# Kernel optimization log

Measured on AMD Instinct MI355X. Metric: run time of the kernel, lower is better.

## Reference

```python
import jax, jax.numpy as jnp
import numpy as np

N, C, E, H = 50000, 128, 1_600_000, 32
JITTER = 1e-20


def _lin(k, fan_in, fan_out):
    return jax.random.normal(k, (fan_in, fan_out), jnp.float32) / np.sqrt(fan_in)


def setup_inputs() -> dict:
    key = jax.random.key(0)
    ks = jax.random.split(key, 20)
    x = jax.random.normal(ks[0], (N, C), jnp.float32)
    edge_index = jax.random.randint(ks[1], (2, E), 0, N, dtype=jnp.int64)
    inp = {"x": x, "edge_index": edge_index}
    # actor params
    inp["aW"] = _lin(ks[2], C, C); inp["ab"] = jnp.zeros((C,), jnp.float32)
    inp["a1W"] = _lin(ks[3], C, H); inp["a1b"] = jnp.zeros((H,), jnp.float32)
    inp["a2W"] = _lin(ks[4], H, H); inp["a2b"] = jnp.zeros((H,), jnp.float32)
    inp["a3W"] = _lin(ks[5], H, 2); inp["a3b"] = jnp.zeros((2,), jnp.float32)
    # critic params
    inp["cW"] = _lin(ks[6], C, C); inp["cb"] = jnp.zeros((C,), jnp.float32)
    inp["c1W"] = _lin(ks[7], C, H); inp["c1b"] = jnp.zeros((H,), jnp.float32)
    inp["c2W"] = _lin(ks[8], H, H); inp["c2b"] = jnp.zeros((H,), jnp.float32)
    inp["c3W"] = _lin(ks[9], H, 2); inp["c3b"] = jnp.zeros((2,), jnp.float32)
    return inp


def gcn_conv(x, src, dst, W, b):
    """Standard PyG GCNConv: add self-loops, symmetric degree norm, X@W, scatter-add, +bias."""
    n = x.shape[0]
    loop = jnp.arange(n)
    s = jnp.concatenate([src, loop])  # [E+N]
    d = jnp.concatenate([dst, loop])
    deg = jax.ops.segment_sum(jnp.ones_like(d, jnp.float32), d, num_segments=n)
    dinv = jnp.where(deg > 0, jax.lax.rsqrt(deg), 0.0)
    norm = dinv[s] * dinv[d]                     # [E+N]
    h = x @ W                                    # [N, C]
    agg = jax.ops.segment_sum(h[s] * norm[:, None], d, num_segments=n)
    return agg + b


def reference(x, edge_index, aW, ab, a1W, a1b, a2W, a2b, a3W, a3b,
              cW, cb, c1W, c1b, c2W, c2b, c3W, c3b):
    src, dst = edge_index[0], edge_index[1]
    # actor
    h = jax.nn.relu(gcn_conv(x, src, dst, aW, ab)) + x
    h = jax.nn.relu(h @ a1W + a1b)
    h = jax.nn.relu(h @ a2W + a2b)
    a = h @ a3W + a3b                            # [N, 2]
    concentration = jax.nn.softplus(a[:, 0]) + JITTER
    p = jax.nn.softplus(a[:, 1])
    action2_probs = p / jnp.sum(p)
    # critic
    hc = jax.nn.relu(gcn_conv(x, src, dst, cW, cb)) + x
    hc = jnp.sum(hc, axis=0)                     # [C]
    hc = jax.nn.relu(hc @ c1W + c1b)
    hc = jax.nn.relu(hc @ c2W + c2b)
    value = hc @ c3W + c3b                       # [2]
    return (concentration, value, action2_probs)
```

## Files before the change

### kernel.cpp

```cpp
#include <hip/hip_runtime.h>
#include <hip/hip_bf16.h>
#include <hip/hip_fp16.h>
#include <math.h>

#define C 128
#define BCAP 12288

using half8x = __attribute__((ext_vector_type(8))) _Float16;
using half4x = __attribute__((ext_vector_type(4))) _Float16;
using f32x4  = __attribute__((ext_vector_type(4))) float;

__device__ inline float4 h4_to_f4(uint2 u) {
    __half2 p0 = *(__half2*)&u.x;
    __half2 p1 = *(__half2*)&u.y;
    float2 f0 = __half22float2(p0), f1 = __half22float2(p1);
    return make_float4(f0.x, f0.y, f1.x, f1.y);
}

__device__ inline float softplusf(float v) {
    return (v > 20.f) ? v : log1pf(expf(v));
}

__global__ __launch_bounds__(256) void initk(unsigned* gcur, float* colsum, float* pSum) {
    int t = threadIdx.x;
    gcur[t] = 0u;
    if (t < 128) colsum[t] = 0.f;
    if (t == 128) pSum[0] = 0.f;
}

__global__ __launch_bounds__(256) void wtk(const float* __restrict__ aW, const float* __restrict__ cW,
                                           const float* __restrict__ a1W,
                                           __half* __restrict__ wt, __half* __restrict__ a1wt) {
    int idx = blockIdx.x * 256 + threadIdx.x;
    if (idx < 32768) {
        int y = idx >> 14, r = idx & 16383;
        int k = r >> 7, n = r & 127;
        const float* W = y ? cW : aW;
        wt[((size_t)y << 14) + n * 128 + k] = __float2half(W[k * 128 + n]);
    } else if (idx < 36864) {
        int r = idx - 32768;
        int k = r >> 5, n = r & 31;
        a1wt[n * 128 + k] = __float2half(a1W[k * 32 + n]);
    }
}

__global__ __launch_bounds__(256) void bink(const int* __restrict__ ei,
                                            unsigned* __restrict__ gcur,
                                            unsigned* __restrict__ gstage,
                                            int E, int NBKT) {
    __shared__ unsigned raw[6400];
    __shared__ unsigned image[6400];
    __shared__ unsigned cnt[256];
    __shared__ unsigned pref[256];
    __shared__ unsigned cur[256];
    __shared__ unsigned gb[256];
    int t = threadIdx.x, b = blockIdx.x;
    int elo = (int)((long long)b * E / 256);
    int ehi = (int)((long long)(b + 1) * E / 256);
    int n = ehi - elo;

    for (int i = t; i < n; i += 256) {
        int d = __builtin_nontemporal_load(ei + E + elo + i);
        int s = __builtin_nontemporal_load(ei + elo + i);
        raw[i] = (unsigned)s | ((unsigned)(d & 255) << 16) | ((unsigned)(d >> 8) << 24);
    }
    cnt[t] = 0u; cur[t] = 0u;
    __syncthreads();
    for (int i = t; i < n; i += 256) atomicAdd(&cnt[raw[i] >> 24], 1u);
    __syncthreads();
    pref[t] = cnt[t];
    __syncthreads();
    for (int off = 1; off < 256; off <<= 1) {
        unsigned add = (t >= off) ? pref[t - off] : 0u;
        __syncthreads();
        pref[t] += add;
        __syncthreads();
    }
    gb[t] = (t < NBKT && cnt[t]) ? atomicAdd(&gcur[t], cnt[t]) : 0u;
    __syncthreads();
    for (int i = t; i < n; i += 256) {
        unsigned v = raw[i];
        unsigned B = v >> 24;
        unsigned pos = (pref[B] - cnt[B]) + atomicAdd(&cur[B], 1u);
        image[pos] = v & 0xFFFFFFu;
    }
    __syncthreads();
    int wv = t >> 6, lane = t & 63;
    for (int B = wv; B < NBKT; B += 4) {
        unsigned c = cnt[B];
        if (!c) continue;
        unsigned eb = pref[B] - c;
        unsigned gbase = gb[B];
        unsigned c2 = (gbase < BCAP) ? ((c < BCAP - gbase) ? c : BCAP - gbase) : 0u;
        for (unsigned i = lane; i < c2; i += 64)
            gstage[(size_t)B * BCAP + gbase + i] = image[eb + i];
    }
}

__global__ void bktscank(const unsigned* __restrict__ gcur, unsigned* __restrict__ bktbase, int NBKT) {
    __shared__ unsigned tmp[256];
    int t = threadIdx.x;
    unsigned g = (t < NBKT) ? gcur[t] : 0u;
    unsigned v = (g < BCAP) ? g : BCAP;
    tmp[t] = v;
    __syncthreads();
    for (int off = 1; off < 256; off <<= 1) {
        unsigned add = (t >= off) ? tmp[t - off] : 0u;
        __syncthreads();
        tmp[t] += add;
        __syncthreads();
    }
    if (t < NBKT) bktbase[t] = tmp[t] - v;
}

__global__ __launch_bounds__(256) void placek(const unsigned* __restrict__ gstage,
                                              const unsigned* __restrict__ gcur,
                                              const unsigned* __restrict__ bktbase,
                                              int* __restrict__ rowptr, float* __restrict__ dinv,
                                              int* __restrict__ col, int N, int NBKT) {
    __shared__ unsigned image[BCAP];
    __shared__ unsigned cnt[256];
    __shared__ unsigned pref[256];
    __shared__ unsigned cur[256];
    int B = blockIdx.x, t = threadIdx.x;
    unsigned g = gcur[B];
    unsigned m = (g < BCAP) ? g : BCAP;
    unsigned base = bktbase[B];
    const unsigned* st = gstage + (size_t)B * BCAP;

    cnt[t] = 0u; cur[t] = 0u;
    __syncthreads();
    for (unsigned i = t; i < m; i += 256) atomicAdd(&cnt[(st[i] >> 16) & 255u], 1u);
    __syncthreads();
    pref[t] = cnt[t];
    __syncthreads();
    for (int off = 1; off < 256; off <<= 1) {
        unsigned add = (t >= off) ? pref[t - off] : 0u;
        __syncthreads();
        pref[t] += add;
        __syncthreads();
    }
    int d = B * 256 + t;
    if (d < N) {
        rowptr[d] = (int)(base + pref[t] - cnt[t]);
        dinv[d] = rsqrtf((float)(cnt[t] + 1u));
    }
    if (B == NBKT - 1 && t == 0) rowptr[N] = (int)(base + m);
    for (unsigned i = t; i < m; i += 256) {
        unsigned v = st[i];
        unsigned dl = (v >> 16) & 255u;
        unsigned pos = (pref[dl] - cnt[dl]) + atomicAdd(&cur[dl], 1u);
        image[pos] = v & 0xFFFFu;
    }
    __syncthreads();
    for (unsigned i = t; i < m; i += 256) col[base + i] = (int)image[i];
}

__global__ __launch_bounds__(256) void xhk(const float* __restrict__ x, const float* __restrict__ dinv,
                                           __half* __restrict__ xh, __half* __restrict__ x16, int N) {
    int i = blockIdx.x * 256 + threadIdx.x;
    if (i >= N * 64) return;
    int node = i >> 6, fp = (i & 63) * 2;
    float w = dinv[node];
    float2 f = *(const float2*)&x[(size_t)node * C + fp];
    __half2 h = __floats2half2_rn(f.x * w, f.y * w);
    __half2 hx = __floats2half2_rn(f.x, f.y);
    *(unsigned*)&xh[(size_t)node * C + fp] = *(unsigned*)&h;
    *(unsigned*)&x16[(size_t)node * C + fp] = *(unsigned*)&hx;
}

__global__ __launch_bounds__(256) void gatherk(const int* __restrict__ col,
                                               const int* __restrict__ rowptr,
                                               const __half* __restrict__ xh,
                                               const float* __restrict__ dinv,
                                               __half* __restrict__ gg, int N) {
    __shared__ int snb[4][64];
    int t = threadIdx.x;
    int wid = t >> 6, lane = t & 63;
    int d = blockIdx.x * 4 + wid;
    if (d >= N) return;
    int beg = rowptr[d], end = rowptr[d + 1];
    int half = lane >> 5, sub = lane & 31;
    int f = sub * 4;

    float a0 = 0.f, a1 = 0.f, a2 = 0.f, a3 = 0.f;

    for (int c = beg; c < end; c += 64) {
        if (c + lane < end) snb[wid][lane] = col[c + lane];
        int n = end - c; if (n > 64) n = 64;
        int j = 0;
        for (; j + 3 < n; j += 4) {
            size_t i0 = (size_t)snb[wid][j + half] * C + f;
            size_t i1 = (size_t)snb[wid][j + 2 + half] * C + f;
            float4 v0 = h4_to_f4(*(const uint2*)&xh[i0]);
            float4 v1 = h4_to_f4(*(const uint2*)&xh[i1]);
            a0 += v0.x + v1.x;
            a1 += v0.y + v1.y;
            a2 += v0.z + v1.z;
            a3 += v0.w + v1.w;
        }
        for (; j < n; j += 2) {
            if (j + half < n) {
                float4 v = h4_to_f4(*(const uint2*)&xh[(size_t)snb[wid][j + half] * C + f]);
                a0 += v.x; a1 += v.y; a2 += v.z; a3 += v.w;
            }
        }
    }
    a0 += __shfl_xor(a0, 32, 64);
    a1 += __shfl_xor(a1, 32, 64);
    a2 += __shfl_xor(a2, 32, 64);
    a3 += __shfl_xor(a3, 32, 64);

    if (half == 0) {
        float4 s4 = h4_to_f4(*(const uint2*)&xh[(size_t)d * C + f]);
        float dv = dinv[d];
        __half2 h0 = __floats2half2_rn((a0 + s4.x) * dv, (a1 + s4.y) * dv);
        __half2 h1 = __floats2half2_rn((a2 + s4.z) * dv, (a3 + s4.w) * dv);
        uint2 u; u.x = *(unsigned*)&h0; u.y = *(unsigned*)&h1;
        *(uint2*)&gg[(size_t)d * C + f] = u;
    }
}

__global__ __launch_bounds__(256) void gemm2k(const __half* __restrict__ gg,
                                              const __half* __restrict__ wt,
                                              const __half* __restrict__ a1wt,
                                              const float* __restrict__ ab, const float* __restrict__ cb,
                                              const __half* __restrict__ x16,
                                              const float* __restrict__ a1b,
                                              const float* __restrict__ a2W, const float* __restrict__ a2b,
                                              const float* __restrict__ a3W, const float* __restrict__ a3b,
                                              float* __restrict__ scratch,
                                              float* __restrict__ out, float* __restrict__ pSum, int N) {
    __shared__ char As[16384];
    __shared__ char Aux[10240];
    _Float16* w2t = (_Float16*)Aux;
    _Float16* h1b = (_Float16*)(Aux + 2560);
    float* w3s    = (float*)(Aux + 7680);
    float* scol   = (float*)(Aux + 7936);

    const int row0 = blockIdx.x * 64;
    const int t = threadIdx.x;

#pragma unroll
    for (int i = 0; i < 4; ++i) {
        int c = t + i * 256;
        int row = c >> 4, cb16 = (c & 15) * 16;
        int grow = row0 + row;
        uint4 u = make_uint4(0u, 0u, 0u, 0u);
        if (grow < N) u = *(const uint4*)&gg[(size_t)grow * C + (c & 15) * 8];
        *(uint4*)(As + row * 256 + (cb16 ^ ((row & 7) << 4))) = u;
    }
#pragma unroll
    for (int i = 0; i < 4; ++i) {
        int idx = t + i * 256;
        int k = idx >> 5, n = idx & 31;
        w2t[n * 40 + k] = (_Float16)a2W[idx];
    }
    if (t < 64) w3s[t] = a3W[t];
    __syncthreads();

    int wv = t >> 6, l = t & 63;
    int lm = l & 15, lk = l >> 4;
    int koffB = lk * 16;
    int koffH = lk * 8;

    const int rowA = wv * 16 + lm;
    const int grow = row0 + rowA;
    const bool valid = grow < N;
    const int sw = (rowA & 7) << 4;

    half8x af[4];
    {
        const char* rp = As + rowA * 256;
#pragma unroll
        for (int kc = 0; kc < 4; ++kc)
            af[kc] = *(const half8x*)(rp + ((kc * 64 + koffB) ^ sw));
    }

    const __half* WA = wt;
    const __half* WC = wt + 16384;

    half8x bfA[4], bfC[4];
    {
        const __half* wpA = WA + lm * 128;
        const __half* wpC = WC + lm * 128;
#pragma unroll
        for (int kc = 0; kc < 4; ++kc) {
            bfA[kc] = *(const half8x*)(wpA + kc * 32 + koffH);
            bfC[kc] = *(const half8x*)(wpC + kc * 32 + koffH);
        }
    }

#pragma unroll
    for (int nc = 0; nc < 8; ++nc) {
        half8x nA[4], nC[4];
        if (nc < 7) {
            const __half* wpA = WA + ((nc + 1) * 16 + lm) * 128;
            const __half* wpC = WC + ((nc + 1) * 16 + lm) * 128;
#pragma unroll
            for (int kc = 0; kc < 4; ++kc) {
                nA[kc] = *(const half8x*)(wpA + kc * 32 + koffH);
                nC[kc] = *(const half8x*)(wpC + kc * 32 + koffH);
            }
        }
        f32x4 accA = {0.f, 0.f, 0.f, 0.f};
        f32x4 accC = {0.f, 0.f, 0.f, 0.f};
#pragma unroll
        for (int kc = 0; kc < 4; ++kc) {
            accA = __builtin_amdgcn_mfma_f32_16x16x32_f16(bfA[kc], af[kc], accA, 0, 0, 0);
            accC = __builtin_amdgcn_mfma_f32_16x16x32_f16(bfC[kc], af[kc], accC, 0, 0, 0);
        }
        float4 bvA = *(const float4*)&ab[nc * 16 + lk * 4];
        float4 bvC = *(const float4*)&cb[nc * 16 + lk * 4];
        half4x xq = {};
        if (valid) xq = *(const half4x*)&x16[(size_t)grow * C + nc * 16 + lk * 4];
        {
            half4x hv = { (_Float16)(valid ? fmaxf(accA[0] + bvA.x, 0.f) + (float)xq[0] : 0.f),
                          (_Float16)(valid ? fmaxf(accA[1] + bvA.y, 0.f) + (float)xq[1] : 0.f),
                          (_Float16)(valid ? fmaxf(accA[2] + bvA.z, 0.f) + (float)xq[2] : 0.f),
                          (_Float16)(valid ? fmaxf(accA[3] + bvA.w, 0.f) + (float)xq[3] : 0.f) };
            *(half4x*)(As + rowA * 256 + ((nc * 32 + lk * 8) ^ sw)) = hv;
        }
        {
            float v0 = valid ? fmaxf(accC[0] + bvC.x, 0.f) + (float)xq[0] : 0.f;
            float v1 = valid ? fmaxf(accC[1] + bvC.y, 0.f) + (float)xq[1] : 0.f;
            float v2 = valid ? fmaxf(accC[2] + bvC.z, 0.f) + (float)xq[2] : 0.f;
            float v3 = valid ? fmaxf(accC[3] + bvC.w, 0.f) + (float)xq[3] : 0.f;
            v0 += __shfl_xor(v0, 1, 64); v0 += __shfl_xor(v0, 2, 64);
            v0 += __shfl_xor(v0, 4, 64); v0 += __shfl_xor(v0, 8, 64);
            v1 += __shfl_xor(v1, 1, 64); v1 += __shfl_xor(v1, 2, 64);
            v1 += __shfl_xor(v1, 4, 64); v1 += __shfl_xor(v1, 8, 64);
            v2 += __shfl_xor(v2, 1, 64); v2 += __shfl_xor(v2, 2, 64);
            v2 += __shfl_xor(v2, 4, 64); v2 += __shfl_xor(v2, 8, 64);
            v3 += __shfl_xor(v3, 1, 64); v3 += __shfl_xor(v3, 2, 64);
            v3 += __shfl_xor(v3, 4, 64); v3 += __shfl_xor(v3, 8, 64);
            if (lm == 0)
                *(float4*)&scol[wv * 128 + nc * 16 + lk * 4] = make_float4(v0, v1, v2, v3);
        }
        if (nc < 7) {
#pragma unroll
            for (int kc = 0; kc < 4; ++kc) { bfA[kc] = nA[kc]; bfC[kc] = nC[kc]; }
        }
    }
    __syncthreads();

    if (t < 128)
        scratch[(size_t)blockIdx.x * 128 + t] = scol[t] + scol[128 + t] + scol[256 + t] + scol[384 + t];

    half8x a1f[4];
    {
        const char* rp = As + rowA * 256;
#pragma unroll
        for (int kc = 0; kc < 4; ++kc)
            a1f[kc] = *(const half8x*)(rp + ((kc * 64 + koffB) ^ sw));
    }
#pragma unroll
    for (int ct = 0; ct < 2; ++ct) {
        const __half* ap = a1wt + (ct * 16 + lm) * 128;
        f32x4 acc1 = {0.f, 0.f, 0.f, 0.f};
#pragma unroll
        for (int kc = 0; kc < 4; ++kc) {
            half8x bq = *(const half8x*)(ap + kc * 32 + koffH);
            acc1 = __builtin_amdgcn_mfma_f32_16x16x32_f16(bq, a1f[kc], acc1, 0, 0, 0);
        }
        float4 b1v = *(const float4*)&a1b[ct * 16 + lk * 4];
        half4x h = { (_Float16)fmaxf(acc1[0] + b1v.x, 0.f),
                     (_Float16)fmaxf(acc1[1] + b1v.y, 0.f),
                     (_Float16)fmaxf(acc1[2] + b1v.z, 0.f),
                     (_Float16)fmaxf(acc1[3] + b1v.w, 0.f) };
        *(half4x*)((char*)h1b + rowA * 80 + ct * 32 + lk * 8) = h;
    }

    half4x alo = *(const half4x*)((char*)h1b + rowA * 80 + lk * 16);
    half4x ahi = *(const half4x*)((char*)h1b + rowA * 80 + lk * 16 + 8);
    half8x a2f = __builtin_shufflevector(alo, ahi, 0, 1, 2, 3, 4, 5, 6, 7);
    float p0 = 0.f, p1 = 0.f;
#pragma unroll
    for (int ct = 0; ct < 2; ++ct) {
        half4x blo = *(const half4x*)((char*)w2t + (ct * 16 + lm) * 80 + lk * 16);
        half4x bhi = *(const half4x*)((char*)w2t + (ct * 16 + lm) * 80 + lk * 16 + 8);
        half8x b2f = __builtin_shufflevector(blo, bhi, 0, 1, 2, 3, 4, 5, 6, 7);
        f32x4 acc2 = {0.f, 0.f, 0.f, 0.f};
        acc2 = __builtin_amdgcn_mfma_f32_16x16x32_f16(b2f, a2f, acc2, 0, 0, 0);
        float4 b2v = *(const float4*)&a2b[ct * 16 + lk * 4];
#pragma unroll
        for (int j = 0; j < 4; ++j) {
            int f = ct * 16 + lk * 4 + j;
            float h2v = fmaxf(acc2[j] + (&b2v.x)[j], 0.f);
            float2 w3 = *(const float2*)&w3s[f * 2];
            p0 += h2v * w3.x;
            p1 += h2v * w3.y;
        }
    }
    p0 += __shfl_xor(p0, 16, 64); p0 += __shfl_xor(p0, 32, 64);
    p1 += __shfl_xor(p1, 16, 64); p1 += __shfl_xor(p1, 32, 64);
    float wave_psum = 0.f;
    if (lk == 0 && valid) {
        float s0 = softplusf(p0 + a3b[0]);
        float s1 = softplusf(p1 + a3b[1]);
        out[grow] = s0 + 1e-20f;
        out[(size_t)N + 2 + grow] = s1;
        wave_psum = s1;
    }
    wave_psum += __shfl_xor(wave_psum, 1, 64);
    wave_psum += __shfl_xor(wave_psum, 2, 64);
    wave_psum += __shfl_xor(wave_psum, 4, 64);
    wave_psum += __shfl_xor(wave_psum, 8, 64);
    wave_psum += __shfl_xor(wave_psum, 16, 64);
    wave_psum += __shfl_xor(wave_psum, 32, 64);
    if (l == 0) atomicAdd(pSum, wave_psum);
}

__global__ __launch_bounds__(128) void csredk(const float* __restrict__ scratch, float* __restrict__ colsum, int nblk) {
    int t = threadIdx.x;
    float s = 0.f;
    for (int b = blockIdx.x; b < nblk; b += gridDim.x)
        s += scratch[(size_t)b * 128 + t];
    atomicAdd(&colsum[t], s);
}

__global__ void critick(const float* __restrict__ colsum,
                        const float* __restrict__ c1W, const float* __restrict__ c1b,
                        const float* __restrict__ c2W, const float* __restrict__ c2b,
                        const float* __restrict__ c3W, const float* __restrict__ c3b,
                        float* __restrict__ out, int N) {
    __shared__ float s1[32], s2[32];
    int t = threadIdx.x;
    if (t < 32) {
        float acc = c1b[t];
        for (int k = 0; k < 128; ++k) acc += colsum[k] * c1W[k * 32 + t];
        s1[t] = fmaxf(acc, 0.f);
    }
    __syncthreads();
    if (t < 32) {
        float acc = c2b[t];
        for (int k = 0; k < 32; ++k) acc += s1[k] * c2W[k * 32 + t];
        s2[t] = fmaxf(acc, 0.f);
    }
    __syncthreads();
    if (t < 2) {
        float acc = c3b[t];
        for (int k = 0; k < 32; ++k) acc += s2[k] * c3W[k * 2 + t];
        out[(size_t)N + t] = acc;
    }
}

__global__ __launch_bounds__(256) void normk(float* __restrict__ out, const float* __restrict__ pSum, int N) {
    int i = blockIdx.x * 256 + threadIdx.x;
    if (i < N) out[(size_t)N + 2 + i] /= pSum[0];
}

extern "C" void kernel_launch(void* const* d_in, const int* in_sizes, int n_in,
                              void* d_out, int out_size, void* d_ws, size_t ws_size,
                              hipStream_t stream) {
    const float* x   = (const float*)d_in[0];
    const int* ei    = (const int*)d_in[1];
    const float* aW  = (const float*)d_in[2];
    const float* ab  = (const float*)d_in[3];
    const float* a1W = (const float*)d_in[4];
    const float* a1b = (const float*)d_in[5];
    const float* a2W = (const float*)d_in[6];
    const float* a2b = (const float*)d_in[7];
    const float* a3W = (const float*)d_in[8];
    const float* a3b = (const float*)d_in[9];
    const float* cW  = (const float*)d_in[10];
    const float* cb  = (const float*)d_in[11];
    const float* c1W = (const float*)d_in[12];
    const float* c1b = (const float*)d_in[13];
    const float* c2W = (const float*)d_in[14];
    const float* c2b = (const float*)d_in[15];
    const float* c3W = (const float*)d_in[16];
    const float* c3b = (const float*)d_in[17];

    const int N = in_sizes[0] / C;
    const int E = in_sizes[1] / 2;
    const int NBKT = (N + 255) / 256;
    const int nblk64 = (N + 63) / 64;
    float* out = (float*)d_out;

    char* ws = (char*)d_ws;
    size_t off = 0;
    auto alloc = [&](size_t bytes) {
        size_t o = off;
        off = (off + bytes + 255) & ~(size_t)255;
        return (void*)(ws + o);
    };
    unsigned* gcur    = (unsigned*)alloc(256 * 4);
    unsigned* bktbase = (unsigned*)alloc(256 * 4);
    unsigned* gstage  = (unsigned*)alloc((size_t)NBKT * BCAP * 4);
    int* rowptr       = (int*)alloc((size_t)(N + 1) * 4);
    float* dinv       = (float*)alloc((size_t)N * 4);
    int* colidx       = (int*)alloc((size_t)E * 4);
    __half* xh        = (__half*)alloc((size_t)N * C * 2);
    __half* x16       = (__half*)alloc((size_t)N * C * 2);
    __half* gg        = (__half*)alloc((size_t)N * C * 2);
    __half* wt        = (__half*)alloc(2 * 16384 * 2);
    __half* a1wt      = (__half*)alloc(4096 * 2);
    float* scratch    = (float*)alloc((size_t)nblk64 * 128 * 4);
    float* colsum     = (float*)alloc(128 * 4);
    float* pSum       = (float*)alloc(4);

    initk<<<1, 256, 0, stream>>>(gcur, colsum, pSum);
    wtk<<<144, 256, 0, stream>>>(aW, cW, a1W, wt, a1wt);
    bink<<<256, 256, 0, stream>>>(ei, gcur, gstage, E, NBKT);
    bktscank<<<1, 256, 0, stream>>>(gcur, bktbase, NBKT);
    placek<<<NBKT, 256, 0, stream>>>(gstage, gcur, bktbase, rowptr, dinv, colidx, N, NBKT);
    xhk<<<(N * 64 + 255) / 256, 256, 0, stream>>>(x, dinv, xh, x16, N);
    gatherk<<<(N + 3) / 4, 256, 0, stream>>>(colidx, rowptr, xh, dinv, gg, N);
    gemm2k<<<nblk64, 256, 0, stream>>>(gg, wt, a1wt, ab, cb, x16,
                                       a1b, a2W, a2b, a3W, a3b,
                                       scratch, out, pSum, N);
    csredk<<<8, 128, 0, stream>>>(scratch, colsum, nblk64);
    critick<<<1, 64, 0, stream>>>(colsum, c1W, c1b, c2W, c2b, c3W, c3b, out, N);
    normk<<<(N + 255) / 256, 256, 0, stream>>>(out, pSum, N);
}
```

Measured before the change: 228.1 us.

## Split gemm2 output columns across waves instead of rows to cut weight loads

In gemm2k, each wave used to own 16 rows and loop over all 8 column chunks, which meant every wave streamed the full WA and WC weight matrices from global memory. Now each wave owns 2 column chunks and loops over all 64 rows, so each wave loads only a quarter of the weights, and A fragments are read from LDS inside the loop. The result goes into a separate Act LDS buffer to avoid read/write conflicts on As. This raises LDS use and LDS reads per wave, and it drops the software prefetch of the next weight chunk.

New measurement: 217.7 us. 1.05x faster.

```diff
diff --git a/kernel.cpp b/kernel.cpp
--- a/kernel.cpp
+++ b/kernel.cpp
@@ -232,7 +232,8 @@
                                               float* __restrict__ scratch,
                                               float* __restrict__ out, float* __restrict__ pSum, int N) {
     __shared__ char As[16384];
-    __shared__ char Aux[10240];
+    __shared__ char Act[16384];
+    __shared__ char Aux[8448];
     _Float16* w2t = (_Float16*)Aux;
     _Float16* h1b = (_Float16*)(Aux + 2560);
     float* w3s    = (float*)(Aux + 7680);
@@ -264,95 +265,78 @@
     int koffB = lk * 16;
     int koffH = lk * 8;
 
-    const int rowA = wv * 16 + lm;
-    const int grow = row0 + rowA;
-    const bool valid = grow < N;
-    const int sw = (rowA & 7) << 4;
-
-    half8x af[4];
-    {
-        const char* rp = As + rowA * 256;
-#pragma unroll
-        for (int kc = 0; kc < 4; ++kc)
-            af[kc] = *(const half8x*)(rp + ((kc * 64 + koffB) ^ sw));
-    }
-
     const __half* WA = wt;
     const __half* WC = wt + 16384;
 
-    half8x bfA[4], bfC[4];
-    {
-        const __half* wpA = WA + lm * 128;
-        const __half* wpC = WC + lm * 128;
+#pragma unroll
+    for (int nc2 = 0; nc2 < 2; ++nc2) {
+        const int nc = wv * 2 + nc2;
+        const __half* wpA = WA + (nc * 16 + lm) * 128;
+        const __half* wpC = WC + (nc * 16 + lm) * 128;
+        half8x bfA[4], bfC[4];
 #pragma unroll
         for (int kc = 0; kc < 4; ++kc) {
             bfA[kc] = *(const half8x*)(wpA + kc * 32 + koffH);
             bfC[kc] = *(const half8x*)(wpC + kc * 32 + koffH);
         }
-    }
-
-#pragma unroll
-    for (int nc = 0; nc < 8; ++nc) {
-        half8x nA[4], nC[4];
-        if (nc < 7) {
-            const __half* wpA = WA + ((nc + 1) * 16 + lm) * 128;
-            const __half* wpC = WC + ((nc + 1) * 16 + lm) * 128;
-#pragma unroll
-            for (int kc = 0; kc < 4; ++kc) {
-                nA[kc] = *(const half8x*)(wpA + kc * 32 + koffH);
-                nC[kc] = *(const half8x*)(wpC + kc * 32 + koffH);
-            }
-        }
-        f32x4 accA = {0.f, 0.f, 0.f, 0.f};
-        f32x4 accC = {0.f, 0.f, 0.f, 0.f};
-#pragma unroll
-        for (int kc = 0; kc < 4; ++kc) {
-            accA = __builtin_amdgcn_mfma_f32_16x16x32_f16(bfA[kc], af[kc], accA, 0, 0, 0);
-            accC = __builtin_amdgcn_mfma_f32_16x16x32_f16(bfC[kc], af[kc], accC, 0, 0, 0);
-        }
         float4 bvA = *(const float4*)&ab[nc * 16 + lk * 4];
         float4 bvC = *(const float4*)&cb[nc * 16 + lk * 4];
-        half4x xq = {};
-        if (valid) xq = *(const half4x*)&x16[(size_t)grow * C + nc * 16 + lk * 4];
-        {
+        float v0 = 0.f, v1 = 0.f, v2 = 0.f, v3 = 0.f;
+
+#pragma unroll
+        for (int rg = 0; rg < 4; ++rg) {
+            int rowA = rg * 16 + lm;
+            int grow = row0 + rowA;
+            bool valid = grow < N;
+            int sw = (rowA & 7) << 4;
+            const char* rp = As + rowA * 256;
+            f32x4 accA = {0.f, 0.f, 0.f, 0.f};
+            f32x4 accC = {0.f, 0.f, 0.f, 0.f};
+#pragma unroll
+            for (int kc = 0; kc < 4; ++kc) {
+                half8x afr = *(const half8x*)(rp + ((kc * 64 + koffB) ^ sw));
+                accA = __builtin_amdgcn_mfma_f32_16x16x32_f16(bfA[kc], afr, accA, 0, 0, 0);
+                accC = __builtin_amdgcn_mfma_f32_16x16x32_f16(bfC[kc], afr, accC, 0, 0, 0);
+            }
+            half4x xq = {};
+            if (valid) xq = *(const half4x*)&x16[(size_t)grow * C + nc * 16 + lk * 4];
             half4x hv = { (_Float16)(valid ? fmaxf(accA[0] + bvA.x, 0.f) + (float)xq[0] : 0.f),
                           (_Float16)(valid ? fmaxf(accA[1] + bvA.y, 0.f) + (float)xq[1] : 0.f),
                           (_Float16)(valid ? fmaxf(accA[2] + bvA.z, 0.f) + (float)xq[2] : 0.f),
                           (_Float16)(valid ? fmaxf(accA[3] + bvA.w, 0.f) + (float)xq[3] : 0.f) };
-            *(half4x*)(As + rowA * 256 + ((nc * 32 + lk * 8) ^ sw)) = hv;
+            *(half4x*)(Act + rowA * 256 + ((nc * 32 + lk * 8) ^ sw)) = hv;
+            v0 += valid ? fmaxf(accC[0] + bvC.x, 0.f) + (float)xq[0] : 0.f;
+            v1 += valid ? fmaxf(accC[1] + bvC.y, 0.f) + (float)xq[1] : 0.f;
+            v2 += valid ? fmaxf(accC[2] + bvC.z, 0.f) + (float)xq[2] : 0.f;
+            v3 += valid ? fmaxf(accC[3] + bvC.w, 0.f) + (float)xq[3] : 0.f;
         }
-        {
-            float v0 = valid ? fmaxf(accC[0] + bvC.x, 0.f) + (float)xq[0] : 0.f;
-            float v1 = valid ? fmaxf(accC[1] + bvC.y, 0.f) + (float)xq[1] : 0.f;
-            float v2 = valid ? fmaxf(accC[2] + bvC.z, 0.f) + (float)xq[2] : 0.f;
-            float v3 = valid ? fmaxf(accC[3] + bvC.w, 0.f) + (float)xq[3] : 0.f;
-            v0 += __shfl_xor(v0, 1, 64); v0 += __shfl_xor(v0, 2, 64);
-            v0 += __shfl_xor(v0, 4, 64); v0 += __shfl_xor(v0, 8, 64);
-            v1 += __shfl_xor(v1, 1, 64); v1 += __shfl_xor(v1, 2, 64);
-            v1 += __shfl_xor(v1, 4, 64); v1 += __shfl_xor(v1, 8, 64);
-            v2 += __shfl_xor(v2, 1, 64); v2 += __shfl_xor(v2, 2, 64);
-            v2 += __shfl_xor(v2, 4, 64); v2 += __shfl_xor(v2, 8, 64);
-            v3 += __shfl_xor(v3, 1, 64); v3 += __shfl_xor(v3, 2, 64);
-            v3 += __shfl_xor(v3, 4, 64); v3 += __shfl_xor(v3, 8, 64);
-            if (lm == 0)
-                *(float4*)&scol[wv * 128 + nc * 16 + lk * 4] = make_float4(v0, v1, v2, v3);
-        }
-        if (nc < 7) {
-#pragma unroll
-            for (int kc = 0; kc < 4; ++kc) { bfA[kc] = nA[kc]; bfC[kc] = nC[kc]; }
-        }
+        v0 += __shfl_xor(v0, 1, 64); v0 += __shfl_xor(v0, 2, 64);
+        v0 += __shfl_xor(v0, 4, 64); v0 += __shfl_xor(v0, 8, 64);
+        v1 += __shfl_xor(v1, 1, 64); v1 += __shfl_xor(v1, 2, 64);
+        v1 += __shfl_xor(v1, 4, 64); v1 += __shfl_xor(v1, 8, 64);
+        v2 += __shfl_xor(v2, 1, 64); v2 += __shfl_xor(v2, 2, 64);
+        v2 += __shfl_xor(v2, 4, 64); v2 += __shfl_xor(v2, 8, 64);
+        v3 += __shfl_xor(v3, 1, 64); v3 += __shfl_xor(v3, 2, 64);
+        v3 += __shfl_xor(v3, 4, 64); v3 += __shfl_xor(v3, 8, 64);
+        if (lm == 0)
+            *(float4*)&scol[nc * 16 + lk * 4] = make_float4(v0, v1, v2, v3);
     }
     __syncthreads();
 
     if (t < 128)
-        scratch[(size_t)blockIdx.x * 128 + t] = scol[t] + scol[128 + t] + scol[256 + t] + scol[384 + t];
+        scratch[(size_t)blockIdx.x * 128 + t] = scol[t];
+
+    const int rowM = wv * 16 + lm;
+    const int growM = row0 + rowM;
+    const bool validM = growM < N;
+    const int swM = (rowM & 7) << 4;
 
     half8x a1f[4];
     {
-        const char* rp = As + rowA * 256;
+        const char* rp = Act + rowM * 256;
 #pragma unroll
         for (int kc = 0; kc < 4; ++kc)
-            a1f[kc] = *(const half8x*)(rp + ((kc * 64 + koffB) ^ sw));
+            a1f[kc] = *(const half8x*)(rp + ((kc * 64 + koffB) ^ swM));
     }
 #pragma unroll
     for (int ct = 0; ct < 2; ++ct) {
@@ -368,11 +352,11 @@
                      (_Float16)fmaxf(acc1[1] + b1v.y, 0.f),
                      (_Float16)fmaxf(acc1[2] + b1v.z, 0.f),
                      (_Float16)fmaxf(acc1[3] + b1v.w, 0.f) };
-        *(half4x*)((char*)h1b + rowA * 80 + ct * 32 + lk * 8) = h;
-    }
-
-    half4x alo = *(const half4x*)((char*)h1b + rowA * 80 + lk * 16);
-    half4x ahi = *(const half4x*)((char*)h1b + rowA * 80 + lk * 16 + 8);
+        *(half4x*)((char*)h1b + rowM * 80 + ct * 32 + lk * 8) = h;
+    }
+
+    half4x alo = *(const half4x*)((char*)h1b + rowM * 80 + lk * 16);
+    half4x ahi = *(const half4x*)((char*)h1b + rowM * 80 + lk * 16 + 8);
     half8x a2f = __builtin_shufflevector(alo, ahi, 0, 1, 2, 3, 4, 5, 6, 7);
     float p0 = 0.f, p1 = 0.f;
 #pragma unroll
@@ -395,11 +379,11 @@
     p0 += __shfl_xor(p0, 16, 64); p0 += __shfl_xor(p0, 32, 64);
     p1 += __shfl_xor(p1, 16, 64); p1 += __shfl_xor(p1, 32, 64);
     float wave_psum = 0.f;
-    if (lk == 0 && valid) {
+    if (lk == 0 && validM) {
         float s0 = softplusf(p0 + a3b[0]);
         float s1 = softplusf(p1 + a3b[1]);
-        out[grow] = s0 + 1e-20f;
-        out[(size_t)N + 2 + grow] = s1;
+        out[growM] = s0 + 1e-20f;
+        out[(size_t)N + 2 + growM] = s1;
         wave_psum = s1;
     }
     wave_psum += __shfl_xor(wave_psum, 1, 64);
```
